# Performance work log

Hardware: AMD Instinct MI355X
Metric: run time of the kernel (lower is better)

## Reference

```python
import jax, jax.numpy as jnp
import numpy as np

B, S, D, DA, DP = 32, 4096, 256, 128, 64


def setup_inputs() -> dict:
    key = jax.random.key(0)
    ks = jax.random.split(key, 10)
    scale = 0.05
    return {
        "h": jax.random.normal(ks[0], (B, S, D), jnp.float32),
        "q": jax.random.normal(ks[1], (B, D), jnp.float32),
        "pf1": jax.random.normal(ks[2], (B, S, DP), jnp.float32),
        "pf2": jax.random.normal(ks[3], (B, S, DP), jnp.float32),
        "Wh": jax.random.normal(ks[4], (DA, D), jnp.float32) * scale,
        "Wq": jax.random.normal(ks[5], (DA, D), jnp.float32) * scale,
        "Wp1": jax.random.normal(ks[6], (DP, DP), jnp.float32) * scale,
        "Wp2": jax.random.normal(ks[7], (DP, DP), jnp.float32) * scale,
        "Wc": jax.random.normal(ks[8], (1, 2 * DA + 2 * DP), jnp.float32) * scale,
        "bc": jax.random.normal(ks[9], (1,), jnp.float32) * scale,
    }


def reference(h, q, pf1, pf2, Wh, Wq, Wp1, Wp2, Wc, bc):
    # h: [B,S,d], q: [B,d], pf1/pf2: [B,S,dp]
    da = Wh.shape[0]
    dp = Wp1.shape[0]
    w = Wc[0]  # [2da+2dp]
    wa, wq, wp1, wp2 = (w[:da], w[da:2 * da], w[2 * da:2 * da + dp], w[2 * da + dp:])
    # context_linear(cat([h_lin, q_lin, pf1_lin, pf2_lin])) decomposes into a sum
    # of per-branch contributions; fuse the two chained matmuls per branch.
    score = (
        h @ (Wh.T @ wa)                 # [B,S]
        + (q @ (Wq.T @ wq))[:, None]    # [B,1] broadcast
        + pf1 @ (Wp1.T @ wp1)           # [B,S]
        + pf2 @ (Wp2.T @ wp2)           # [B,S]
        + bc[0]
    )
    values = jnp.tanh(score)            # dropout is identity in eval
    att = jax.nn.softmax(values, axis=-1)  # [B,S]
    # torch.mean over the stacked S axis -> weighted MEAN, not sum
    context = jnp.einsum('bs,bsd->bd', att, h) / h.shape[1]
    return context
```

## Files before the change

### kernel.cpp

```cpp
#include <hip/hip_runtime.h>
#include <math.h>

#define BB 32
#define SS 4096
#define DD 256
#define DAA 128
#define DPP 64
#define CHUNKS 64
#define ROWS_PER_BLOCK (SS / CHUNKS)
#define WAVES_PER_BLOCK 4
#define ROWS_PER_WAVE (ROWS_PER_BLOCK / WAVES_PER_BLOCK)
#define BATCH 8
#define NBATCH (ROWS_PER_WAVE / BATCH)
#define VH_SLICES 8
#define SLICE (DAA / VH_SLICES)

#define WS_VHP  0
#define WS_VQP  (WS_VHP + VH_SLICES*DD)
#define WS_VP   (WS_VQP + VH_SLICES*DD)
#define WS_BC   (WS_VP + 128)
#define WS_PART (WS_BC + 16)
#define PART_STRIDE 258

typedef float f4 __attribute__((ext_vector_type(4)));
typedef float f2 __attribute__((ext_vector_type(2)));

__global__ void prep_kernel(const float* __restrict__ Wh,
                            const float* __restrict__ Wq,
                            const float* __restrict__ Wp1,
                            const float* __restrict__ Wp2,
                            const float* __restrict__ Wc,
                            const float* __restrict__ bc,
                            float* __restrict__ ws) {
    const int tid = threadIdx.x;
    const int blk = blockIdx.x;
    if (blk < VH_SLICES) {
        const int a0 = blk * SLICE;
        float vh = 0.f, vq = 0.f;
        #pragma unroll
        for (int i = 0; i < SLICE; ++i) {
            const int a = a0 + i;
            vh += Wh[a * DD + tid] * Wc[a];
            vq += Wq[a * DD + tid] * Wc[DAA + a];
        }
        ws[WS_VHP + blk * DD + tid] = vh;
        ws[WS_VQP + blk * DD + tid] = vq;
    } else {
        if (tid < DPP) {
            float vp1 = 0.f, vp2 = 0.f;
            for (int a = 0; a < DPP; ++a) {
                vp1 += Wp1[a * DPP + tid] * Wc[2 * DAA + a];
                vp2 += Wp2[a * DPP + tid] * Wc[2 * DAA + DPP + a];
            }
            ws[WS_VP + tid]       = vp1;
            ws[WS_VP + DPP + tid] = vp2;
        }
        if (tid == 0) ws[WS_BC] = bc[0];
    }
}

__global__ __launch_bounds__(256, 6) void
main_kernel(const float* __restrict__ h,
            const float* __restrict__ q,
            const float* __restrict__ pf1,
            const float* __restrict__ pf2,
            float* __restrict__ ws) {
    const int c    = blockIdx.x;
    const int b    = blockIdx.y;
    const int tid  = threadIdx.x;
    const int wave = tid >> 6;
    const int lane = tid & 63;
    const int ll   = lane & 31;

    f4 vh4 = {0.f, 0.f, 0.f, 0.f};
    f4 vq4 = {0.f, 0.f, 0.f, 0.f};
    #pragma unroll
    for (int k = 0; k < VH_SLICES; ++k) {
        vh4 += ((const f4*)(ws + WS_VHP + k * DD))[lane];
        vq4 += ((const f4*)(ws + WS_VQP + k * DD))[lane];
    }
    const f2 vpl = ((const f2*)(ws + WS_VP))[lane];

    const float4 q4 = ((const float4*)(q + (size_t)b * DD))[lane];
    float qp = q4.x * vq4.x + q4.y * vq4.y + q4.z * vq4.z + q4.w * vq4.w;
    #pragma unroll
    for (int off = 32; off >= 1; off >>= 1) qp += __shfl_xor(qp, off, 64);
    const float qd = qp + ws[WS_BC];

    const int s0 = c * ROWS_PER_BLOCK + wave * ROWS_PER_WAVE;
    const f4*    hbase = (const f4*)(h + (size_t)b * SS * DD);
    const float* pfsel = ((lane < 32) ? pf1 : pf2) + (size_t)b * SS * DPP + 2 * ll;

    float  l = 0.f;
    float4 ctx = make_float4(0.f, 0.f, 0.f, 0.f);

    for (int ib = 0; ib < NBATCH; ++ib) {
        const int sb = s0 + ib * BATCH;
        f4    h4[BATCH];
        f2    pv[BATCH];
        float part[BATCH];
        #pragma unroll
        for (int j = 0; j < BATCH; ++j) {
            const int s = sb + j;
            h4[j] = __builtin_nontemporal_load(hbase + (size_t)s * (DD / 4) + lane);
            pv[j] = __builtin_nontemporal_load((const f2*)(pfsel + (size_t)s * DPP));
        }
        #pragma unroll
        for (int j = 0; j < BATCH; ++j) {
            part[j] = h4[j].x * vh4.x + h4[j].y * vh4.y
                    + h4[j].z * vh4.z + h4[j].w * vh4.w
                    + pv[j].x * vpl.x + pv[j].y * vpl.y;
        }
        #pragma unroll
        for (int off = 32; off >= 1; off >>= 1) {
            #pragma unroll
            for (int j = 0; j < BATCH; ++j)
                part[j] += __shfl_xor(part[j], off, 64);
        }
        #pragma unroll
        for (int j = 0; j < BATCH; ++j) {
            const float score = part[j] + qd;
            const float e2 = __expf(2.f * score);
            const float t  = 1.f - 2.f * __builtin_amdgcn_rcpf(e2 + 1.f);
            const float w  = __expf(t);
            l += w;
            ctx.x += w * h4[j].x;
            ctx.y += w * h4[j].y;
            ctx.z += w * h4[j].z;
            ctx.w += w * h4[j].w;
        }
    }

    __shared__ float s_l[WAVES_PER_BLOCK];
    __shared__ float s_ctx[WAVES_PER_BLOCK][DD];
    if (lane == 0) s_l[wave] = l;
    ((float4*)s_ctx[wave])[lane] = ctx;
    __syncthreads();

    const float cd = s_ctx[0][tid] + s_ctx[1][tid] + s_ctx[2][tid] + s_ctx[3][tid];
    float* part_out = ws + WS_PART + (size_t)(b * CHUNKS + c) * PART_STRIDE;
    part_out[1 + tid] = cd;
    if (tid == 0) part_out[0] = s_l[0] + s_l[1] + s_l[2] + s_l[3];
}

__global__ void finalize_kernel(const float* __restrict__ ws,
                                float* __restrict__ out) {
    const int b   = blockIdx.x;
    const int tid = threadIdx.x;
    __shared__ float s_l[CHUNKS];
    const float* base = ws + WS_PART + (size_t)b * CHUNKS * PART_STRIDE;
    if (tid < CHUNKS) s_l[tid] = base[(size_t)tid * PART_STRIDE];
    __syncthreads();
    float L = 0.f, acc = 0.f;
    #pragma unroll 8
    for (int c = 0; c < CHUNKS; ++c) {
        L   += s_l[c];
        acc += base[(size_t)c * PART_STRIDE + 1 + tid];
    }
    out[b * DD + tid] = acc / (L * (float)SS);
}

extern "C" void kernel_launch(void* const* d_in, const int* in_sizes, int n_in,
                              void* d_out, int out_size, void* d_ws, size_t ws_size,
                              hipStream_t stream) {
    const float* h   = (const float*)d_in[0];
    const float* q   = (const float*)d_in[1];
    const float* pf1 = (const float*)d_in[2];
    const float* pf2 = (const float*)d_in[3];
    const float* Wh  = (const float*)d_in[4];
    const float* Wq  = (const float*)d_in[5];
    const float* Wp1 = (const float*)d_in[6];
    const float* Wp2 = (const float*)d_in[7];
    const float* Wc  = (const float*)d_in[8];
    const float* bc  = (const float*)d_in[9];
    float* out = (float*)d_out;
    float* ws  = (float*)d_ws;

    prep_kernel<<<VH_SLICES + 1, 256, 0, stream>>>(Wh, Wq, Wp1, Wp2, Wc, bc, ws);
    main_kernel<<<dim3(CHUNKS, BB), 256, 0, stream>>>(h, q, pf1, pf2, ws);
    finalize_kernel<<<BB, 256, 0, stream>>>(ws, out);
}
```

Before: 245.3 us.

## Double-buffer row batches in main kernel and halve chunk count

Replaces the batch loop with an explicit two-buffer software pipeline, so the next batch of h and pf rows is being loaded while the current batch is reduced. Chunks per batch row drop from 64 to 32, giving each wave 32 rows (four batches) and fewer partials to finalize. The launch-bounds occupancy hint drops from 6 to 4 to make room for the doubled register buffers. The risks are fewer blocks in the grid and lower occupancy for latency hiding.

```diff
diff --git a/kernel.cpp b/kernel.cpp
--- a/kernel.cpp
+++ b/kernel.cpp
@@ -6,7 +6,7 @@
 #define DD 256
 #define DAA 128
 #define DPP 64
-#define CHUNKS 64
+#define CHUNKS 32
 #define ROWS_PER_BLOCK (SS / CHUNKS)
 #define WAVES_PER_BLOCK 4
 #define ROWS_PER_WAVE (ROWS_PER_BLOCK / WAVES_PER_BLOCK)
@@ -59,7 +59,46 @@
     }
 }
 
-__global__ __launch_bounds__(256, 6) void
+#define LOADB(H, P, IB)                                                        \
+    {                                                                          \
+        const int sb_ = s0 + (IB) * BATCH;                                     \
+        _Pragma("unroll")                                                      \
+        for (int j = 0; j < BATCH; ++j) {                                      \
+            const int s_ = sb_ + j;                                            \
+            H[j] = __builtin_nontemporal_load(hbase + (size_t)s_ * (DD / 4) + lane); \
+            P[j] = __builtin_nontemporal_load((const f2*)(pfsel + (size_t)s_ * DPP)); \
+        }                                                                      \
+    }
+
+#define COMPUTE(H, P)                                                          \
+    {                                                                          \
+        float part[BATCH];                                                     \
+        _Pragma("unroll")                                                      \
+        for (int j = 0; j < BATCH; ++j)                                        \
+            part[j] = H[j].x * vh4.x + H[j].y * vh4.y                          \
+                    + H[j].z * vh4.z + H[j].w * vh4.w                          \
+                    + P[j].x * vpl.x + P[j].y * vpl.y;                         \
+        _Pragma("unroll")                                                      \
+        for (int off = 32; off >= 1; off >>= 1) {                              \
+            _Pragma("unroll")                                                  \
+            for (int j = 0; j < BATCH; ++j)                                    \
+                part[j] += __shfl_xor(part[j], off, 64);                       \
+        }                                                                      \
+        _Pragma("unroll")                                                      \
+        for (int j = 0; j < BATCH; ++j) {                                      \
+            const float score = part[j] + qd;                                  \
+            const float e2 = __expf(2.f * score);                              \
+            const float t  = 1.f - 2.f * __builtin_amdgcn_rcpf(e2 + 1.f);      \
+            const float w  = __expf(t);                                        \
+            l += w;                                                            \
+            ctx.x += w * H[j].x;                                               \
+            ctx.y += w * H[j].y;                                               \
+            ctx.z += w * H[j].z;                                               \
+            ctx.w += w * H[j].w;                                               \
+        }                                                                      \
+    }
+
+__global__ __launch_bounds__(256, 4) void
 main_kernel(const float* __restrict__ h,
             const float* __restrict__ q,
             const float* __restrict__ pf1,
@@ -94,42 +133,16 @@
     float  l = 0.f;
     float4 ctx = make_float4(0.f, 0.f, 0.f, 0.f);
 
-    for (int ib = 0; ib < NBATCH; ++ib) {
-        const int sb = s0 + ib * BATCH;
-        f4    h4[BATCH];
-        f2    pv[BATCH];
-        float part[BATCH];
-        #pragma unroll
-        for (int j = 0; j < BATCH; ++j) {
-            const int s = sb + j;
-            h4[j] = __builtin_nontemporal_load(hbase + (size_t)s * (DD / 4) + lane);
-            pv[j] = __builtin_nontemporal_load((const f2*)(pfsel + (size_t)s * DPP));
-        }
-        #pragma unroll
-        for (int j = 0; j < BATCH; ++j) {
-            part[j] = h4[j].x * vh4.x + h4[j].y * vh4.y
-                    + h4[j].z * vh4.z + h4[j].w * vh4.w
-                    + pv[j].x * vpl.x + pv[j].y * vpl.y;
-        }
-        #pragma unroll
-        for (int off = 32; off >= 1; off >>= 1) {
-            #pragma unroll
-            for (int j = 0; j < BATCH; ++j)
-                part[j] += __shfl_xor(part[j], off, 64);
-        }
-        #pragma unroll
-        for (int j = 0; j < BATCH; ++j) {
-            const float score = part[j] + qd;
-            const float e2 = __expf(2.f * score);
-            const float t  = 1.f - 2.f * __builtin_amdgcn_rcpf(e2 + 1.f);
-            const float w  = __expf(t);
-            l += w;
-            ctx.x += w * h4[j].x;
-            ctx.y += w * h4[j].y;
-            ctx.z += w * h4[j].z;
-            ctx.w += w * h4[j].w;
-        }
-    }
+    f4 hA[BATCH], hB[BATCH];
+    f2 pA[BATCH], pB[BATCH];
+    LOADB(hA, pA, 0)
+    LOADB(hB, pB, 1)
+    COMPUTE(hA, pA)
+    LOADB(hA, pA, 2)
+    COMPUTE(hB, pB)
+    LOADB(hB, pB, 3)
+    COMPUTE(hA, pA)
+    COMPUTE(hB, pB)
 
     __shared__ float s_l[WAVES_PER_BLOCK];
     __shared__ float s_ctx[WAVES_PER_BLOCK][DD];
```

Result: slower. 285.9 us (+16.6%).

## Double-buffer row batch loads in main kernel with larger per-block chunks

Applied to the files above, without the earlier changes.

Restructures the main loop into an explicitly unrolled ping-pong pipeline: the next batch of h and pf rows is loaded into a second register set while the current batch is reduced and accumulated. Chunks per batch row are halved so each block handles more rows, batch size is halved, and the launch-bounds occupancy hint is lowered to allow more registers. The aim is to hide global memory latency within each wave, at the cost of fewer blocks and possibly fewer resident waves.

```diff
diff --git a/kernel.cpp b/kernel.cpp
--- a/kernel.cpp
+++ b/kernel.cpp
@@ -6,11 +6,11 @@
 #define DD 256
 #define DAA 128
 #define DPP 64
-#define CHUNKS 64
+#define CHUNKS 32
 #define ROWS_PER_BLOCK (SS / CHUNKS)
 #define WAVES_PER_BLOCK 4
 #define ROWS_PER_WAVE (ROWS_PER_BLOCK / WAVES_PER_BLOCK)
-#define BATCH 8
+#define BATCH 4
 #define NBATCH (ROWS_PER_WAVE / BATCH)
 #define VH_SLICES 8
 #define SLICE (DAA / VH_SLICES)
@@ -59,7 +59,7 @@
     }
 }
 
-__global__ __launch_bounds__(256, 6) void
+__global__ __launch_bounds__(256, 4) void
 main_kernel(const float* __restrict__ h,
             const float* __restrict__ q,
             const float* __restrict__ pf1,
@@ -94,23 +94,26 @@
     float  l = 0.f;
     float4 ctx = make_float4(0.f, 0.f, 0.f, 0.f);
 
-    for (int ib = 0; ib < NBATCH; ++ib) {
+    f4 hA[BATCH], hB[BATCH];
+    f2 pA[BATCH], pB[BATCH];
+
+    auto loadb = [&](int ib, f4 (&H)[BATCH], f2 (&P)[BATCH]) {
         const int sb = s0 + ib * BATCH;
-        f4    h4[BATCH];
-        f2    pv[BATCH];
-        float part[BATCH];
         #pragma unroll
         for (int j = 0; j < BATCH; ++j) {
             const int s = sb + j;
-            h4[j] = __builtin_nontemporal_load(hbase + (size_t)s * (DD / 4) + lane);
-            pv[j] = __builtin_nontemporal_load((const f2*)(pfsel + (size_t)s * DPP));
+            H[j] = __builtin_nontemporal_load(hbase + (size_t)s * (DD / 4) + lane);
+            P[j] = __builtin_nontemporal_load((const f2*)(pfsel + (size_t)s * DPP));
         }
+    };
+
+    auto compute = [&](f4 (&H)[BATCH], f2 (&P)[BATCH]) {
+        float part[BATCH];
         #pragma unroll
-        for (int j = 0; j < BATCH; ++j) {
-            part[j] = h4[j].x * vh4.x + h4[j].y * vh4.y
-                    + h4[j].z * vh4.z + h4[j].w * vh4.w
-                    + pv[j].x * vpl.x + pv[j].y * vpl.y;
-        }
+        for (int j = 0; j < BATCH; ++j)
+            part[j] = H[j].x * vh4.x + H[j].y * vh4.y
+                    + H[j].z * vh4.z + H[j].w * vh4.w
+                    + P[j].x * vpl.x + P[j].y * vpl.y;
         #pragma unroll
         for (int off = 32; off >= 1; off >>= 1) {
             #pragma unroll
@@ -124,12 +127,23 @@
             const float t  = 1.f - 2.f * __builtin_amdgcn_rcpf(e2 + 1.f);
             const float w  = __expf(t);
             l += w;
-            ctx.x += w * h4[j].x;
-            ctx.y += w * h4[j].y;
-            ctx.z += w * h4[j].z;
-            ctx.w += w * h4[j].w;
+            ctx.x += w * H[j].x;
+            ctx.y += w * H[j].y;
+            ctx.z += w * H[j].z;
+            ctx.w += w * H[j].w;
         }
-    }
+    };
+
+    loadb(0, hA, pA);
+    loadb(1, hB, pB);
+    compute(hA, pA);  loadb(2, hA, pA);
+    compute(hB, pB);  loadb(3, hB, pB);
+    compute(hA, pA);  loadb(4, hA, pA);
+    compute(hB, pB);  loadb(5, hB, pB);
+    compute(hA, pA);  loadb(6, hA, pA);
+    compute(hB, pB);  loadb(7, hB, pB);
+    compute(hA, pA);
+    compute(hB, pB);
 
     __shared__ float s_l[WAVES_PER_BLOCK];
     __shared__ float s_ctx[WAVES_PER_BLOCK][DD];
```

Result: slower. 270.3 us (+10.2%).
